# Performance work log

Hardware: AMD Instinct MI355X
Metric: run time of the kernel (lower is better)

## Reference

```python
import jax, jax.numpy as jnp
import numpy as np

N_NODES = 50000
N_EDGES = 800000
F_IN = 128
LN_EPS = 1e-5


def _linear_params(key, fan_in, fan_out):
    kw, kb = jax.random.split(key)
    w = jax.random.normal(kw, (fan_in, fan_out), dtype=jnp.float32) * 0.02
    b = jax.random.normal(kb, (fan_out,), dtype=jnp.float32) * 0.02
    return w, b


def setup_inputs() -> dict:
    key = jax.random.key(0)
    ks = jax.random.split(key, 16)
    x = jax.random.normal(ks[0], (N_NODES, F_IN), dtype=jnp.float32)
    edge_index = jax.random.randint(ks[1], (2, N_EDGES), 0, N_NODES, dtype=jnp.int32)
    w1a, b1a = _linear_params(ks[2], F_IN, 256)
    w1b, b1b = _linear_params(ks[3], 256, 256)
    w2a, b2a = _linear_params(ks[4], 256, 512)
    w2b, b2b = _linear_params(ks[5], 512, 512)
    w3a, b3a = _linear_params(ks[6], 512, 1024)
    w3b, b3b = _linear_params(ks[7], 1024, 1024)
    rp1_w, rp1_b = _linear_params(ks[8], F_IN, 256)
    rp2_w, rp2_b = _linear_params(ks[9], 256, 512)
    rp3_w, rp3_b = _linear_params(ks[10], 512, 1024)
    ln1_g = jnp.ones((256,), jnp.float32); ln1_b = jnp.zeros((256,), jnp.float32)
    ln2_g = jnp.ones((512,), jnp.float32); ln2_b = jnp.zeros((512,), jnp.float32)
    ln3_g = jnp.ones((1024,), jnp.float32); ln3_b = jnp.zeros((1024,), jnp.float32)
    return dict(x=x, edge_index=edge_index,
                w1a=w1a, b1a=b1a, w1b=w1b, b1b=b1b,
                w2a=w2a, b2a=b2a, w2b=w2b, b2b=b2b,
                w3a=w3a, b3a=b3a, w3b=w3b, b3b=b3b,
                rp1_w=rp1_w, rp1_b=rp1_b, rp2_w=rp2_w, rp2_b=rp2_b,
                rp3_w=rp3_w, rp3_b=rp3_b,
                ln1_g=ln1_g, ln1_b=ln1_b, ln2_g=ln2_g, ln2_b=ln2_b,
                ln3_g=ln3_g, ln3_b=ln3_b)


def _layer_norm(h, g, b):
    mu = jnp.mean(h, axis=-1, keepdims=True)
    var = jnp.mean(jnp.square(h - mu), axis=-1, keepdims=True)
    return (h - mu) * jax.lax.rsqrt(var + LN_EPS) * g + b


def _gin_conv(h, src, dst, wa, ba, wb, bb):
    # GINConv with eps=0: mlp(x_i + sum_{j->i} x_j), scatter-add at targets
    agg = jax.ops.segment_sum(h[src], dst, num_segments=N_NODES)
    z = h + agg
    z = jax.nn.relu(z @ wa + ba)
    z = jax.nn.relu(z @ wb + bb)
    return z


def _forward(x, edge_index,
             w1a, b1a, w1b, b1b, w2a, b2a, w2b, b2b, w3a, b3a, w3b, b3b,
             rp1_w, rp1_b, rp2_w, rp2_b, rp3_w, rp3_b,
             ln1_g, ln1_b, ln2_g, ln2_b, ln3_g, ln3_b):
    src, dst = edge_index[0], edge_index[1]
    # block 1
    res = x @ rp1_w + rp1_b
    h = _gin_conv(x, src, dst, w1a, b1a, w1b, b1b)
    h = jax.nn.relu(h + res)          # dropout = identity in eval
    h = _layer_norm(h, ln1_g, ln1_b)
    # block 2
    res = h @ rp2_w + rp2_b
    h2 = _gin_conv(h, src, dst, w2a, b2a, w2b, b2b)
    h = jax.nn.relu(h2 + res)
    h = _layer_norm(h, ln2_g, ln2_b)
    # block 3
    res = h @ rp3_w + rp3_b
    h3 = _gin_conv(h, src, dst, w3a, b3a, w3b, b3b)
    h = jax.nn.relu(h3 + res)
    h = _layer_norm(h, ln3_g, ln3_b)
    return h


def reference(x, edge_index,
              w1a, b1a, w1b, b1b, w2a, b2a, w2b, b2b, w3a, b3a, w3b, b3b,
              rp1_w, rp1_b, rp2_w, rp2_b, rp3_w, rp3_b,
              ln1_g, ln1_b, ln2_g, ln2_b, ln3_g, ln3_b):
    return _forward(x, edge_index,
                    w1a, b1a, w1b, b1b, w2a, b2a, w2b, b2b, w3a, b3a, w3b, b3b,
                    rp1_w, rp1_b, rp2_w, rp2_b, rp3_w, rp3_b,
                    ln1_g, ln1_b, ln2_g, ln2_b, ln3_g, ln3_b)
```

## Files before the change

kernel.cpp:

```cpp
#include <hip/hip_runtime.h>
#include <stdint.h>

#define NN 50000
#define NE 800000
#define M_PAD 50048

typedef __attribute__((ext_vector_type(8))) short short8;
typedef __attribute__((ext_vector_type(4))) float f32x4;

static __device__ __forceinline__ float bf2f(unsigned short v) {
    union { unsigned u; float f; } c; c.u = ((unsigned)v) << 16; return c.f;
}
static __device__ __forceinline__ unsigned short f2bf(float f) {
    union { float f; unsigned u; } c; c.f = f;
    unsigned u = c.u;
    u += 0x7fffu + ((u >> 16) & 1u);
    return (unsigned short)(u >> 16);
}

__global__ void f32_to_bf16_k(const float* __restrict__ in, unsigned short* __restrict__ out, long n4) {
    long i = (long)blockIdx.x * 256 + threadIdx.x;
    if (i >= n4) return;
    float4 v = ((const float4*)in)[i];
    ushort4 o; o.x = f2bf(v.x); o.y = f2bf(v.y); o.z = f2bf(v.z); o.w = f2bf(v.w);
    ((ushort4*)out)[i] = o;
}
__global__ void wt_k(const float* __restrict__ w, unsigned short* __restrict__ wt, int K, int N) {
    int i = blockIdx.x * 256 + threadIdx.x;
    if (i >= K * N) return;
    int k = i % K, n = i / K;
    wt[i] = f2bf(w[(long)k * N + n]);
}

__global__ void zero_k(int* __restrict__ p, int n) {
    int i = blockIdx.x * 256 + threadIdx.x;
    if (i < n) p[i] = 0;
}
__global__ void hist_k(const int* __restrict__ ei, int* __restrict__ deg) {
    int e = blockIdx.x * 256 + threadIdx.x;
    if (e >= NE) return;
    atomicAdd(&deg[ei[NE + e]], 1);
}
__global__ __launch_bounds__(1024)
void scan_k(const int* __restrict__ deg, int* __restrict__ row_ptr, int* __restrict__ cursor) {
    constexpr int T = 1024, C = (NN + T - 1) / T;
    const int tid = threadIdx.x;
    const int base = tid * C;
    int s = 0;
#pragma unroll 4
    for (int i = 0; i < C; ++i) {
        int idx = base + i;
        if (idx < NN) s += deg[idx];
    }
    __shared__ int sm[T];
    sm[tid] = s;
    __syncthreads();
    for (int off = 1; off < T; off <<= 1) {
        int v = (tid >= off) ? sm[tid - off] : 0;
        __syncthreads();
        sm[tid] += v;
        __syncthreads();
    }
    int run = (tid == 0) ? 0 : sm[tid - 1];
#pragma unroll 4
    for (int i = 0; i < C; ++i) {
        int idx = base + i;
        if (idx < NN) {
            row_ptr[idx] = run;
            cursor[idx] = run;
            run += deg[idx];
        }
    }
}
__global__ void build_col_k(const int* __restrict__ ei, int* __restrict__ cursor, int* __restrict__ col) {
    int e = blockIdx.x * 256 + threadIdx.x;
    if (e >= NE) return;
    int d = ei[NE + e];
    int p = atomicAdd(&cursor[d], 1);
    col[p] = ei[e];
}

template <int V> struct VecT;
template <> struct VecT<2> { using T = unsigned int; };
template <> struct VecT<4> { using T = uint2; };
template <> struct VecT<8> { using T = uint4; };

template <int D>
__global__ __launch_bounds__(256)
void agg_gather_k(const unsigned short* __restrict__ h,
                  const int* __restrict__ row_ptr, const int* __restrict__ deg,
                  const int* __restrict__ col, unsigned short* __restrict__ z) {
    constexpr int V = D / 64;
    using VT = typename VecT<V>::T;
    union U { VT v; unsigned short s[V]; };
    const int node = blockIdx.x * 4 + (threadIdx.x >> 6);
    if (node >= NN) return;
    const int lane = threadIdx.x & 63;
    const size_t fb = (size_t)lane * V;

    float acc[V];
    {
        U b; b.v = *(const VT*)(h + (size_t)node * D + fb);
#pragma unroll
        for (int i = 0; i < V; ++i) acc[i] = bf2f(b.s[i]);
    }
    const int s = row_ptr[node];
    const int e = s + deg[node];
    int t = s;
    for (; t + 2 <= e; t += 2) {
        int s0 = col[t], s1 = col[t + 1];
        U a0, a1;
        a0.v = *(const VT*)(h + (size_t)s0 * D + fb);
        a1.v = *(const VT*)(h + (size_t)s1 * D + fb);
#pragma unroll
        for (int i = 0; i < V; ++i) acc[i] += bf2f(a0.s[i]);
#pragma unroll
        for (int i = 0; i < V; ++i) acc[i] += bf2f(a1.s[i]);
    }
    if (t < e) {
        U a; a.v = *(const VT*)(h + (size_t)col[t] * D + fb);
#pragma unroll
        for (int i = 0; i < V; ++i) acc[i] += bf2f(a.s[i]);
    }
    U o;
#pragma unroll
    for (int i = 0; i < V; ++i) o.s[i] = f2bf(acc[i]);
    *(VT*)(z + (size_t)node * D + fb) = o.v;
}

static __device__ __forceinline__ void stage_tile128x64(
    const unsigned short* __restrict__ src, size_t rstride,
    unsigned short* lds, int wid, int lane) {
#pragma unroll
    for (int r = 0; r < 4; ++r) {
        const int rows8 = wid * 32 + r * 8;
        const int row = rows8 + (lane >> 3);
        const int kblk = (lane & 7) ^ (row & 7);
        __builtin_amdgcn_global_load_lds(
            (const __attribute__((address_space(1))) void*)(src + (size_t)row * rstride + (size_t)kblk * 8),
            (__attribute__((address_space(3))) void*)(lds + rows8 * 64),
            16, 0, 0);
    }
}

#define GEMM_IDS                                   \
    const int tid = threadIdx.x;                   \
    const int lane = tid & 63;                     \
    const int wid = tid >> 6;                      \
    const int wm = wid & 1, wn = wid >> 1;         \
    const int l15 = lane & 15, quad = lane >> 4;   \
    const int m0 = blockIdx.y * 128;               \
    const int n0 = blockIdx.x * 128;

#define GEMM_KSTEP(AP, BP, KS)                                                        \
    for (int k0 = 0; k0 < (KS); k0 += 64) {                                           \
        stage_tile128x64((AP) + (size_t)m0 * (KS) + k0, (KS), lA, wid, lane);         \
        stage_tile128x64((BP) + (size_t)n0 * (KS) + k0, (KS), lB, wid, lane);         \
        __syncthreads();                                                              \
        _Pragma("unroll")                                                             \
        for (int kk = 0; kk < 2; ++kk) {                                              \
            short8 aF[4], bF[4];                                                      \
            _Pragma("unroll")                                                         \
            for (int i = 0; i < 4; ++i) {                                             \
                int ml = wm * 64 + i * 16 + l15;                                      \
                int kb = kk * 4 + quad;                                               \
                aF[i] = *(const short8*)&lA[(ml * 8 + (kb ^ (ml & 7))) * 8];          \
                int nl = wn * 64 + i * 16 + l15;                                      \
                bF[i] = *(const short8*)&lB[(nl * 8 + (kb ^ (nl & 7))) * 8];          \
            }                                                                         \
            _Pragma("unroll")                                                         \
            for (int i = 0; i < 4; ++i)                                               \
                _Pragma("unroll")                                                     \
                for (int j = 0; j < 4; ++j)                                           \
                    acc[i][j] = __builtin_amdgcn_mfma_f32_16x16x32_bf16(              \
                        aF[i], bF[j], acc[i][j], 0, 0, 0);                            \
        }                                                                             \
        __syncthreads();                                                              \
    }

template <int K, int N>
__global__ __launch_bounds__(256, 2)
void gemm_relu_k(const unsigned short* __restrict__ A, const unsigned short* __restrict__ Bt,
                 const float* __restrict__ bias, unsigned short* __restrict__ outH, int M) {
    __shared__ unsigned short lA[128 * 64];
    __shared__ unsigned short lB[128 * 64];
    GEMM_IDS
    f32x4 acc[4][4];
#pragma unroll
    for (int i = 0; i < 4; ++i)
#pragma unroll
        for (int j = 0; j < 4; ++j) acc[i][j] = (f32x4){0.f, 0.f, 0.f, 0.f};

    GEMM_KSTEP(A, Bt, K)

#pragma unroll
    for (int i = 0; i < 4; ++i) {
#pragma unroll
        for (int j = 0; j < 4; ++j) {
            int col = n0 + wn * 64 + j * 16 + l15;
            float bv = bias[col];
#pragma unroll
            for (int r = 0; r < 4; ++r) {
                int row = m0 + wm * 64 + i * 16 + quad * 4 + r;
                if (row < M)
                    outH[(size_t)row * N + col] = f2bf(fmaxf(acc[i][j][r] + bv, 0.f));
            }
        }
    }
}

template <int K1, int K2, int N>
__global__ __launch_bounds__(256, 2)
void gemm_fused_k(const unsigned short* __restrict__ A1, const unsigned short* __restrict__ B1t,
                  const float* __restrict__ b1,
                  const unsigned short* __restrict__ A2, const unsigned short* __restrict__ B2t,
                  const float* __restrict__ b2,
                  float* __restrict__ outF, int M) {
    __shared__ unsigned short lA[128 * 64];
    __shared__ unsigned short lB[128 * 64];
    GEMM_IDS
    f32x4 acc[4][4];
#pragma unroll
    for (int i = 0; i < 4; ++i)
#pragma unroll
        for (int j = 0; j < 4; ++j) acc[i][j] = (f32x4){0.f, 0.f, 0.f, 0.f};

    GEMM_KSTEP(A1, B1t, K1)

#pragma unroll
    for (int j = 0; j < 4; ++j) {
        float bv = b1[n0 + wn * 64 + j * 16 + l15];
#pragma unroll
        for (int i = 0; i < 4; ++i)
#pragma unroll
            for (int r = 0; r < 4; ++r)
                acc[i][j][r] = fmaxf(acc[i][j][r] + bv, 0.f);
    }

    GEMM_KSTEP(A2, B2t, K2)

#pragma unroll
    for (int i = 0; i < 4; ++i) {
#pragma unroll
        for (int j = 0; j < 4; ++j) {
            int col = n0 + wn * 64 + j * 16 + l15;
            float bv = b2[col];
#pragma unroll
            for (int r = 0; r < 4; ++r) {
                int row = m0 + wm * 64 + i * 16 + quad * 4 + r;
                if (row < M)
                    outF[(size_t)row * N + col] = fmaxf(acc[i][j][r] + bv, 0.f);
            }
        }
    }
}

template <int D, bool BF16OUT>
__global__ __launch_bounds__(256)
void ln_k(const float* __restrict__ t, const float* __restrict__ g, const float* __restrict__ b,
          unsigned short* __restrict__ outH, float* __restrict__ outF) {
    constexpr int VPT = D / 256;
    const int row = blockIdx.x;
    const int tid = threadIdx.x;
    const float* tp = t + (size_t)row * D;
    float vals[VPT];
    float s = 0.f, ss = 0.f;
#pragma unroll
    for (int i = 0; i < VPT; ++i) {
        float v = tp[i * 256 + tid];
        vals[i] = v; s += v; ss += v * v;
    }
#pragma unroll
    for (int off = 32; off; off >>= 1) { s += __shfl_down(s, off); ss += __shfl_down(ss, off); }
    __shared__ float ps[4], pss[4];
    int lane = tid & 63, wv = tid >> 6;
    if (lane == 0) { ps[wv] = s; pss[wv] = ss; }
    __syncthreads();
    float st = ps[0] + ps[1] + ps[2] + ps[3];
    float sst = pss[0] + pss[1] + pss[2] + pss[3];
    float mean = st / D;
    float var = sst / D - mean * mean;
    float inv = rsqrtf(var + 1e-5f);
#pragma unroll
    for (int i = 0; i < VPT; ++i) {
        int c = i * 256 + tid;
        float o = (vals[i] - mean) * inv * g[c] + b[c];
        if (BF16OUT) outH[(size_t)row * D + c] = f2bf(o);
        else outF[(size_t)row * D + c] = o;
    }
}

static inline int cdiv(long a, long b) { return (int)((a + b - 1) / b); }

extern "C" void kernel_launch(void* const* d_in, const int* in_sizes, int n_in,
                              void* d_out, int out_size, void* d_ws, size_t ws_size,
                              hipStream_t stream) {
    const float* x   = (const float*)d_in[0];
    const int*   ei  = (const int*)  d_in[1];
    const float* w1a = (const float*)d_in[2],  *b1a = (const float*)d_in[3];
    const float* w1b = (const float*)d_in[4],  *b1b = (const float*)d_in[5];
    const float* w2a = (const float*)d_in[6],  *b2a = (const float*)d_in[7];
    const float* w2b = (const float*)d_in[8],  *b2b = (const float*)d_in[9];
    const float* w3a = (const float*)d_in[10], *b3a = (const float*)d_in[11];
    const float* w3b = (const float*)d_in[12], *b3b = (const float*)d_in[13];
    const float* rp1 = (const float*)d_in[14], *rp1b = (const float*)d_in[15];
    const float* rp2 = (const float*)d_in[16], *rp2b = (const float*)d_in[17];
    const float* rp3 = (const float*)d_in[18], *rp3b = (const float*)d_in[19];
    const float* g1 = (const float*)d_in[20], *be1 = (const float*)d_in[21];
    const float* g2 = (const float*)d_in[22], *be2 = (const float*)d_in[23];
    const float* g3 = (const float*)d_in[24], *be3 = (const float*)d_in[25];

    char* ws = (char*)d_ws;
    size_t off = 0;
    auto alloc = [&](size_t n) { char* p = ws + off; off += (n + 255) & ~(size_t)255; return p; };
    unsigned short* w1aT = (unsigned short*)alloc((size_t)128 * 256 * 2);
    unsigned short* w1bT = (unsigned short*)alloc((size_t)256 * 256 * 2);
    unsigned short* w2aT = (unsigned short*)alloc((size_t)256 * 512 * 2);
    unsigned short* w2bT = (unsigned short*)alloc((size_t)512 * 512 * 2);
    unsigned short* w3aT = (unsigned short*)alloc((size_t)512 * 1024 * 2);
    unsigned short* w3bT = (unsigned short*)alloc((size_t)1024 * 1024 * 2);
    unsigned short* rp1T = (unsigned short*)alloc((size_t)128 * 256 * 2);
    unsigned short* rp2T = (unsigned short*)alloc((size_t)256 * 512 * 2);
    unsigned short* rp3T = (unsigned short*)alloc((size_t)512 * 1024 * 2);
    unsigned short* hA  = (unsigned short*)alloc((size_t)M_PAD * 512 * 2);
    unsigned short* hB  = (unsigned short*)alloc((size_t)M_PAD * 512 * 2);
    unsigned short* zin = (unsigned short*)alloc((size_t)M_PAD * 512 * 2);
    unsigned short* z1  = (unsigned short*)alloc((size_t)M_PAD * 1024 * 2);
    float* resb = (float*)alloc((size_t)M_PAD * 1024 * 4);
    int* deg     = (int*)alloc((size_t)NN * 4);
    int* row_ptr = (int*)alloc((size_t)NN * 4);
    int* cursor  = (int*)alloc((size_t)NN * 4);
    int* colv    = (int*)alloc((size_t)NE * 4);
    (void)ws_size; (void)in_sizes; (void)n_in; (void)out_size;

    zero_k<<<cdiv(NN, 256), 256, 0, stream>>>(deg, NN);
    hist_k<<<cdiv(NE, 256), 256, 0, stream>>>(ei, deg);
    scan_k<<<1, 1024, 0, stream>>>(deg, row_ptr, cursor);
    build_col_k<<<cdiv(NE, 256), 256, 0, stream>>>(ei, cursor, colv);

    wt_k<<<cdiv(128 * 256, 256), 256, 0, stream>>>(w1a, w1aT, 128, 256);
    wt_k<<<cdiv(256 * 256, 256), 256, 0, stream>>>(w1b, w1bT, 256, 256);
    wt_k<<<cdiv(256 * 512, 256), 256, 0, stream>>>(w2a, w2aT, 256, 512);
    wt_k<<<cdiv(512 * 512, 256), 256, 0, stream>>>(w2b, w2bT, 512, 512);
    wt_k<<<cdiv(512 * 1024, 256), 256, 0, stream>>>(w3a, w3aT, 512, 1024);
    wt_k<<<cdiv(1024 * 1024, 256), 256, 0, stream>>>(w3b, w3bT, 1024, 1024);
    wt_k<<<cdiv(128 * 256, 256), 256, 0, stream>>>(rp1, rp1T, 128, 256);
    wt_k<<<cdiv(256 * 512, 256), 256, 0, stream>>>(rp2, rp2T, 256, 512);
    wt_k<<<cdiv(512 * 1024, 256), 256, 0, stream>>>(rp3, rp3T, 512, 1024);

    f32_to_bf16_k<<<cdiv((long)NN * 128 / 4, 256), 256, 0, stream>>>(x, hA, (long)NN * 128 / 4);

    agg_gather_k<128><<<cdiv(NN, 4), 256, 0, stream>>>(hA, row_ptr, deg, colv, zin);
    gemm_relu_k<128, 256><<<dim3(2, 391), 256, 0, stream>>>(zin, w1aT, b1a, z1, NN);
    gemm_fused_k<256, 128, 256><<<dim3(2, 391), 256, 0, stream>>>(z1, w1bT, b1b, hA, rp1T, rp1b, resb, NN);
    ln_k<256, true><<<NN, 256, 0, stream>>>(resb, g1, be1, hB, nullptr);

    agg_gather_k<256><<<cdiv(NN, 4), 256, 0, stream>>>(hB, row_ptr, deg, colv, zin);
    gemm_relu_k<256, 512><<<dim3(4, 391), 256, 0, stream>>>(zin, w2aT, b2a, z1, NN);
    gemm_fused_k<512, 256, 512><<<dim3(4, 391), 256, 0, stream>>>(z1, w2bT, b2b, hB, rp2T, rp2b, resb, NN);
    ln_k<512, true><<<NN, 256, 0, stream>>>(resb, g2, be2, hA, nullptr);

    agg_gather_k<512><<<cdiv(NN, 4), 256, 0, stream>>>(hA, row_ptr, deg, colv, zin);
    gemm_relu_k<512, 1024><<<dim3(8, 391), 256, 0, stream>>>(zin, w3aT, b3a, z1, NN);
    gemm_fused_k<1024, 512, 1024><<<dim3(8, 391), 256, 0, stream>>>(z1, w3bT, b3b, hA, rp3T, rp3b, resb, NN);
    ln_k<1024, false><<<NN, 256, 0, stream>>>(resb, g3, be3, nullptr, (float*)d_out);
}
```

Measured before the change: 1.307 ms.

## Replace GEMMs with 256x128 double-buffered 8-wave pipelined MFMA kernel

Replaces the 128x128 single-buffered 4-wave GEMMs with one templated 256x128 tile kernel using 8 waves, double-buffered LDS and staged global_load_lds prefetch. Waits are explicit vmcnt/s_barrier, and MFMA phases run at raised priority so loads overlap compute. Blocks are remapped with XCD-aware swizzling for L2 locality, and M_PAD grows to cover the 256-row tiles. The intent is to hide global-load latency and improve reuse, at the cost of more LDS per block and fragile hand-written wait counts.

```diff
diff --git a/kernel.cpp b/kernel.cpp
--- a/kernel.cpp
+++ b/kernel.cpp
@@ -3,7 +3,7 @@
 
 #define NN 50000
 #define NE 800000
-#define M_PAD 50048
+#define M_PAD 50176
 
 typedef __attribute__((ext_vector_type(8))) short short8;
 typedef __attribute__((ext_vector_type(4))) float f32x4;
@@ -128,128 +128,194 @@
     *(VT*)(z + (size_t)node * D + fb) = o.v;
 }
 
-static __device__ __forceinline__ void stage_tile128x64(
-    const unsigned short* __restrict__ src, size_t rstride,
-    unsigned short* lds, int wid, int lane) {
-#pragma unroll
-    for (int r = 0; r < 4; ++r) {
-        const int rows8 = wid * 32 + r * 8;
-        const int row = rows8 + (lane >> 3);
-        const int kblk = (lane & 7) ^ (row & 7);
-        __builtin_amdgcn_global_load_lds(
-            (const __attribute__((address_space(1))) void*)(src + (size_t)row * rstride + (size_t)kblk * 8),
-            (__attribute__((address_space(3))) void*)(lds + rows8 * 64),
-            16, 0, 0);
-    }
-}
-
-#define GEMM_IDS                                   \
-    const int tid = threadIdx.x;                   \
-    const int lane = tid & 63;                     \
-    const int wid = tid >> 6;                      \
-    const int wm = wid & 1, wn = wid >> 1;         \
-    const int l15 = lane & 15, quad = lane >> 4;   \
-    const int m0 = blockIdx.y * 128;               \
-    const int n0 = blockIdx.x * 128;
-
-#define GEMM_KSTEP(AP, BP, KS)                                                        \
-    for (int k0 = 0; k0 < (KS); k0 += 64) {                                           \
-        stage_tile128x64((AP) + (size_t)m0 * (KS) + k0, (KS), lA, wid, lane);         \
-        stage_tile128x64((BP) + (size_t)n0 * (KS) + k0, (KS), lB, wid, lane);         \
-        __syncthreads();                                                              \
-        _Pragma("unroll")                                                             \
-        for (int kk = 0; kk < 2; ++kk) {                                              \
-            short8 aF[4], bF[4];                                                      \
-            _Pragma("unroll")                                                         \
-            for (int i = 0; i < 4; ++i) {                                             \
-                int ml = wm * 64 + i * 16 + l15;                                      \
-                int kb = kk * 4 + quad;                                               \
-                aF[i] = *(const short8*)&lA[(ml * 8 + (kb ^ (ml & 7))) * 8];          \
-                int nl = wn * 64 + i * 16 + l15;                                      \
-                bF[i] = *(const short8*)&lB[(nl * 8 + (kb ^ (nl & 7))) * 8];          \
-            }                                                                         \
-            _Pragma("unroll")                                                         \
-            for (int i = 0; i < 4; ++i)                                               \
-                _Pragma("unroll")                                                     \
-                for (int j = 0; j < 4; ++j)                                           \
-                    acc[i][j] = __builtin_amdgcn_mfma_f32_16x16x32_bf16(              \
-                        aF[i], bF[j], acc[i][j], 0, 0, 0);                            \
-        }                                                                             \
-        __syncthreads();                                                              \
-    }
-
-template <int K, int N>
-__global__ __launch_bounds__(256, 2)
-void gemm_relu_k(const unsigned short* __restrict__ A, const unsigned short* __restrict__ Bt,
-                 const float* __restrict__ bias, unsigned short* __restrict__ outH, int M) {
-    __shared__ unsigned short lA[128 * 64];
-    __shared__ unsigned short lB[128 * 64];
-    GEMM_IDS
+
+static __device__ __forceinline__ void stg(const unsigned short* src, int rstride,
+                                           unsigned short* ldsb, int row8, int lane) {
+    const int row = row8 + (lane >> 3);
+    const int kblk = (lane & 7) ^ (row & 7);
+    __builtin_amdgcn_global_load_lds(
+        (const __attribute__((address_space(1))) void*)(src + (size_t)row * rstride + (size_t)kblk * 8),
+        (__attribute__((address_space(3))) void*)(ldsb + row8 * 64),
+        16, 0, 0);
+}
+
+#define G_BAR asm volatile("s_barrier" ::: "memory")
+#define WAITV(n) asm volatile("s_waitcnt vmcnt(" #n ")" ::: "memory")
+
+#define ALO_ROW8(g) ((((g) >> 2) << 6) + (((g) & 3) << 3))
+#define AHI_ROW8(g) (ALO_ROW8(g) + 32)
+
+#define PHASE_LOAD(BUF, Q)                                                         \
+    short8 aF[2][2], bF[4][2];                                                     \
+    _Pragma("unroll") for (int kk = 0; kk < 2; ++kk) {                             \
+        const int kb = kk * 4 + quad;                                              \
+        _Pragma("unroll") for (int m2 = 0; m2 < 2; ++m2) {                         \
+            const int ml = wm * 64 + ((Q) * 2 + m2) * 16 + l15;                    \
+            aF[m2][kk] = *(const short8*)&lA[BUF][(ml * 8 + (kb ^ (ml & 7))) * 8]; \
+        }                                                                          \
+        _Pragma("unroll") for (int nj = 0; nj < 4; ++nj) {                         \
+            const int nl = wn * 64 + nj * 16 + l15;                                \
+            bF[nj][kk] = *(const short8*)&lB[BUF][(nl * 8 + (kb ^ (nl & 7))) * 8]; \
+        }                                                                          \
+    }
+
+#define PHASE_MFMA(Q)                                                              \
+    __builtin_amdgcn_s_setprio(1);                                                 \
+    _Pragma("unroll") for (int m2 = 0; m2 < 2; ++m2)                               \
+        _Pragma("unroll") for (int nj = 0; nj < 4; ++nj)                           \
+            _Pragma("unroll") for (int kk = 0; kk < 2; ++kk)                       \
+                acc[(Q) * 2 + m2][nj] = __builtin_amdgcn_mfma_f32_16x16x32_bf16(   \
+                    aF[m2][kk], bF[nj][kk], acc[(Q) * 2 + m2][nj], 0, 0, 0);       \
+    __builtin_amdgcn_s_setprio(0);
+
+template <int K1, int K2, int N, bool FUSED>
+__global__ __launch_bounds__(512, 2)
+void gemm8_k(const unsigned short* __restrict__ A1, const unsigned short* __restrict__ B1t,
+             const float* __restrict__ bias1,
+             const unsigned short* __restrict__ A2, const unsigned short* __restrict__ B2t,
+             const float* __restrict__ bias2,
+             unsigned short* __restrict__ outH, float* __restrict__ outF, int M) {
+    constexpr int NT1 = K1 / 64;
+    constexpr int NT2 = (K2 > 0) ? K2 / 64 : 0;
+    constexpr int NT = NT1 + NT2;
+    constexpr int NI = NT / 2;
+    static_assert(NT % 2 == 0 && NT >= 2, "NT must be even");
+    constexpr int NTn = N / 128;
+
+    __shared__ unsigned short lA[2][256 * 64];
+    __shared__ unsigned short lB[2][128 * 64];
+
+    const int tid = threadIdx.x;
+    const int lane = tid & 63;
+    const int wid = tid >> 6;
+    const int wm = wid >> 1, wn = wid & 1;
+    const int l15 = lane & 15, quad = lane >> 4;
+
+    int m0, n0;
+    {
+        const int nwg = NTn * (int)gridDim.y;
+        const int orig = (int)(blockIdx.y * gridDim.x + blockIdx.x);
+        const int q = nwg >> 3, r = nwg & 7;
+        const int xcd = orig & 7, idx = orig >> 3;
+        const int logical = (xcd < r ? xcd * (q + 1) : r * (q + 1) + (xcd - r) * q) + idx;
+        m0 = (logical / NTn) * 256;
+        n0 = (logical % NTn) * 128;
+    }
+
+    const unsigned short* baseA1 = A1 + (size_t)m0 * K1;
+    const unsigned short* baseB1 = B1t + (size_t)n0 * K1;
+    const unsigned short* baseA2 = FUSED ? A2 + (size_t)m0 * K2 : nullptr;
+    const unsigned short* baseB2 = FUSED ? B2t + (size_t)n0 * K2 : nullptr;
+
+    auto srcA = [&](int t, const unsigned short*& p, int& st) {
+        if (!FUSED || t < NT1) { p = baseA1 + (size_t)t * 64; st = K1; }
+        else                   { p = baseA2 + (size_t)(t - NT1) * 64; st = K2; }
+    };
+    auto srcB = [&](int t, const unsigned short*& p, int& st) {
+        if (!FUSED || t < NT1) { p = baseB1 + (size_t)t * 64; st = K1; }
+        else                   { p = baseB2 + (size_t)(t - NT1) * 64; st = K2; }
+    };
+
     f32x4 acc[4][4];
 #pragma unroll
     for (int i = 0; i < 4; ++i)
 #pragma unroll
         for (int j = 0; j < 4; ++j) acc[i][j] = (f32x4){0.f, 0.f, 0.f, 0.f};
 
-    GEMM_KSTEP(A, Bt, K)
-
-#pragma unroll
-    for (int i = 0; i < 4; ++i) {
-#pragma unroll
-        for (int j = 0; j < 4; ++j) {
-            int col = n0 + wn * 64 + j * 16 + l15;
-            float bv = bias[col];
+    float bmid[4];
+    if constexpr (FUSED) {
+#pragma unroll
+        for (int j = 0; j < 4; ++j) bmid[j] = bias1[n0 + wn * 64 + j * 16 + l15];
+    }
+
+    {
+        const unsigned short* pa; int sa; srcA(0, pa, sa);
+#pragma unroll
+        for (int k = 0; k < 4; ++k) stg(pa, sa, &lA[0][0], (k * 8 + wid) * 8, lane);
+        const unsigned short* pb; int sb; srcB(0, pb, sb);
+#pragma unroll
+        for (int k = 0; k < 2; ++k) stg(pb, sb, &lB[0][0], (k * 8 + wid) * 8, lane);
+        const unsigned short* pa1; int sa1; srcA(1, pa1, sa1);
+        stg(pa1, sa1, &lA[1][0], ALO_ROW8(wid), lane);
+        stg(pa1, sa1, &lA[1][0], ALO_ROW8(8 + wid), lane);
+    }
+
+    for (int i = 0; i < NI; ++i) {
+        const int t0 = 2 * i, t1 = 2 * i + 1;
+        const int tc = (t0 + 2 < NT) ? t0 + 2 : NT - 1;
+        const int tc2 = (t1 + 2 < NT) ? t1 + 2 : NT - 1;
+
+        {
+            const unsigned short* pa; int sa; srcA(t1, pa, sa);
+            stg(pa, sa, &lA[1][0], AHI_ROW8(wid), lane);
+            stg(pa, sa, &lA[1][0], AHI_ROW8(8 + wid), lane);
+            const unsigned short* pb; int sb; srcB(t1, pb, sb);
+            stg(pb, sb, &lB[1][0], wid * 8, lane);
+            stg(pb, sb, &lB[1][0], (8 + wid) * 8, lane);
+        }
+        WAITV(6);
+        G_BAR;
+        { PHASE_LOAD(0, 0); PHASE_MFMA(0); }
+        G_BAR;
+
+        {
+            const unsigned short* pa; int sa; srcA(tc, pa, sa);
+            stg(pa, sa, &lA[0][0], ALO_ROW8(wid), lane);
+            stg(pa, sa, &lA[0][0], ALO_ROW8(8 + wid), lane);
+        }
+        { PHASE_LOAD(0, 1); G_BAR; PHASE_MFMA(1); }
+        G_BAR;
+
+        {
+            const unsigned short* pa; int sa; srcA(tc, pa, sa);
+            stg(pa, sa, &lA[0][0], AHI_ROW8(wid), lane);
+            stg(pa, sa, &lA[0][0], AHI_ROW8(8 + wid), lane);
+            const unsigned short* pb; int sb; srcB(tc, pb, sb);
+            stg(pb, sb, &lB[0][0], wid * 8, lane);
+        }
+        WAITV(5);
+        G_BAR;
+        { PHASE_LOAD(1, 0); PHASE_MFMA(0); }
+        G_BAR;
+
+        {
+            const unsigned short* pb; int sb; srcB(tc, pb, sb);
+            stg(pb, sb, &lB[0][0], (8 + wid) * 8, lane);
+            const unsigned short* pa; int sa; srcA(tc2, pa, sa);
+            stg(pa, sa, &lA[1][0], ALO_ROW8(wid), lane);
+            stg(pa, sa, &lA[1][0], ALO_ROW8(8 + wid), lane);
+        }
+        { PHASE_LOAD(1, 1); G_BAR; PHASE_MFMA(1); }
+        if constexpr (FUSED) {
+            if (i == NT1 / 2 - 1) {
+#pragma unroll
+                for (int jj = 0; jj < 4; ++jj)
+#pragma unroll
+                    for (int ii = 0; ii < 4; ++ii)
+#pragma unroll
+                        for (int rr = 0; rr < 4; ++rr)
+                            acc[ii][jj][rr] = fmaxf(acc[ii][jj][rr] + bmid[jj], 0.f);
+            }
+        }
+        G_BAR;
+    }
+    WAITV(0);
+
+    const float* bfin = FUSED ? bias2 : bias1;
+#pragma unroll
+    for (int j = 0; j < 4; ++j) {
+        const int col = n0 + wn * 64 + j * 16 + l15;
+        const float bv = bfin[col];
+#pragma unroll
+        for (int i = 0; i < 4; ++i) {
 #pragma unroll
             for (int r = 0; r < 4; ++r) {
-                int row = m0 + wm * 64 + i * 16 + quad * 4 + r;
-                if (row < M)
-                    outH[(size_t)row * N + col] = f2bf(fmaxf(acc[i][j][r] + bv, 0.f));
-            }
-        }
-    }
-}
-
-template <int K1, int K2, int N>
-__global__ __launch_bounds__(256, 2)
-void gemm_fused_k(const unsigned short* __restrict__ A1, const unsigned short* __restrict__ B1t,
-                  const float* __restrict__ b1,
-                  const unsigned short* __restrict__ A2, const unsigned short* __restrict__ B2t,
-                  const float* __restrict__ b2,
-                  float* __restrict__ outF, int M) {
-    __shared__ unsigned short lA[128 * 64];
-    __shared__ unsigned short lB[128 * 64];
-    GEMM_IDS
-    f32x4 acc[4][4];
-#pragma unroll
-    for (int i = 0; i < 4; ++i)
-#pragma unroll
-        for (int j = 0; j < 4; ++j) acc[i][j] = (f32x4){0.f, 0.f, 0.f, 0.f};
-
-    GEMM_KSTEP(A1, B1t, K1)
-
-#pragma unroll
-    for (int j = 0; j < 4; ++j) {
-        float bv = b1[n0 + wn * 64 + j * 16 + l15];
-#pragma unroll
-        for (int i = 0; i < 4; ++i)
-#pragma unroll
-            for (int r = 0; r < 4; ++r)
-                acc[i][j][r] = fmaxf(acc[i][j][r] + bv, 0.f);
-    }
-
-    GEMM_KSTEP(A2, B2t, K2)
-
-#pragma unroll
-    for (int i = 0; i < 4; ++i) {
-#pragma unroll
-        for (int j = 0; j < 4; ++j) {
-            int col = n0 + wn * 64 + j * 16 + l15;
-            float bv = b2[col];
-#pragma unroll
-            for (int r = 0; r < 4; ++r) {
-                int row = m0 + wm * 64 + i * 16 + quad * 4 + r;
-                if (row < M)
-                    outF[(size_t)row * N + col] = fmaxf(acc[i][j][r] + bv, 0.f);
+                const int row = m0 + wm * 64 + i * 16 + quad * 4 + r;
+                if (row < M) {
+                    const float v = fmaxf(acc[i][j][r] + bv, 0.f);
+                    if constexpr (FUSED) outF[(size_t)row * N + col] = v;
+                    else outH[(size_t)row * N + col] = f2bf(v);
+                }
             }
         }
     }
@@ -351,17 +417,23 @@
     f32_to_bf16_k<<<cdiv((long)NN * 128 / 4, 256), 256, 0, stream>>>(x, hA, (long)NN * 128 / 4);
 
     agg_gather_k<128><<<cdiv(NN, 4), 256, 0, stream>>>(hA, row_ptr, deg, colv, zin);
-    gemm_relu_k<128, 256><<<dim3(2, 391), 256, 0, stream>>>(zin, w1aT, b1a, z1, NN);
-    gemm_fused_k<256, 128, 256><<<dim3(2, 391), 256, 0, stream>>>(z1, w1bT, b1b, hA, rp1T, rp1b, resb, NN);
+    gemm8_k<128, 0, 256, false><<<dim3(2, 196), 512, 0, stream>>>(
+        zin, w1aT, b1a, nullptr, nullptr, nullptr, z1, nullptr, NN);
+    gemm8_k<256, 128, 256, true><<<dim3(2, 196), 512, 0, stream>>>(
+        z1, w1bT, b1b, hA, rp1T, rp1b, nullptr, resb, NN);
     ln_k<256, true><<<NN, 256, 0, stream>>>(resb, g1, be1, hB, nullptr);
 
     agg_gather_k<256><<<cdiv(NN, 4), 256, 0, stream>>>(hB, row_ptr, deg, colv, zin);
-    gemm_relu_k<256, 512><<<dim3(4, 391), 256, 0, stream>>>(zin, w2aT, b2a, z1, NN);
-    gemm_fused_k<512, 256, 512><<<dim3(4, 391), 256, 0, stream>>>(z1, w2bT, b2b, hB, rp2T, rp2b, resb, NN);
+    gemm8_k<256, 0, 512, false><<<dim3(4, 196), 512, 0, stream>>>(
+        zin, w2aT, b2a, nullptr, nullptr, nullptr, z1, nullptr, NN);
+    gemm8_k<512, 256, 512, true><<<dim3(4, 196), 512, 0, stream>>>(
+        z1, w2bT, b2b, hB, rp2T, rp2b, nullptr, resb, NN);
     ln_k<512, true><<<NN, 256, 0, stream>>>(resb, g2, be2, hA, nullptr);
 
     agg_gather_k<512><<<cdiv(NN, 4), 256, 0, stream>>>(hA, row_ptr, deg, colv, zin);
-    gemm_relu_k<512, 1024><<<dim3(8, 391), 256, 0, stream>>>(zin, w3aT, b3a, z1, NN);
-    gemm_fused_k<1024, 512, 1024><<<dim3(8, 391), 256, 0, stream>>>(z1, w3bT, b3b, hA, rp3T, rp3b, resb, NN);
+    gemm8_k<512, 0, 1024, false><<<dim3(8, 196), 512, 0, stream>>>(
+        zin, w3aT, b3a, nullptr, nullptr, nullptr, z1, nullptr, NN);
+    gemm8_k<1024, 512, 1024, true><<<dim3(8, 196), 512, 0, stream>>>(
+        z1, w3bT, b3b, hA, rp3T, rp3b, nullptr, resb, NN);
     ln_k<1024, false><<<NN, 256, 0, stream>>>(resb, g3, be3, nullptr, (float*)d_out);
 }
```

Result: slower. 1.666 ms (+27.5%).
